# Kernel tuning notes

Measured on AMD Instinct MI355X. Metric: run time of the kernel, lower is better.

## Reference

```python
import jax, jax.numpy as jnp
import numpy as np

D_EMBED = 1024
N_HEADS = 16
BATCH = 2
SEQ = 2048


def setup_inputs() -> dict:
    key = jax.random.key(0)
    k1, k2, k3 = jax.random.split(key, 3)
    scale = 0.02
    x = jax.random.normal(k1, (BATCH, SEQ, D_EMBED), dtype=jnp.float32)
    w_qkv = jax.random.normal(k2, (D_EMBED, 3 * D_EMBED), dtype=jnp.float32) * scale
    b_qkv = jnp.zeros((3 * D_EMBED,), dtype=jnp.float32)
    w_o = jax.random.normal(k3, (D_EMBED, D_EMBED), dtype=jnp.float32) * scale
    b_o = jnp.zeros((D_EMBED,), dtype=jnp.float32)
    return {"x": x, "w_qkv": w_qkv, "b_qkv": b_qkv, "w_o": w_o, "b_o": b_o}


def reference(x, w_qkv, b_qkv, w_o, b_o):
    bs, sl, ed = x.shape
    nh = N_HEADS
    hd = ed // nh
    # fused QKV projection, split into q, k, v
    qkv = x @ w_qkv + b_qkv                      # [bs, sl, 3*ed]
    q, k, v = jnp.split(qkv, 3, axis=2)
    # [bs, sl, (nh hd)] -> [bs, nh, sl, hd]
    def heads(t):
        return t.reshape(bs, sl, nh, hd).transpose(0, 2, 1, 3)
    q, k, v = heads(q), heads(k), heads(v)
    # scaled dot-product attention with causal mask (full SxS scores, as in the original)
    scores = jnp.einsum('bhqd,bhkd->bhqk', q, k) / jnp.sqrt(jnp.float32(hd))
    causal = jnp.tril(jnp.ones((sl, sl), dtype=bool))
    scores = jnp.where(causal[None, None, :, :], scores, jnp.float32(-jnp.inf))
    attn = jax.nn.softmax(scores, axis=-1)       # dropout p=0 -> identity
    out = jnp.einsum('bhqk,bhkd->bhqd', attn, v) # [bs, nh, sl, hd]
    out = out.transpose(0, 2, 1, 3).reshape(bs, sl, ed)
    return out @ w_o + b_o
```

## Files before the change

kernel.cpp:

```cpp
#include <hip/hip_runtime.h>
#include <hip/hip_bf16.h>

typedef __hip_bfloat16 bf16;
typedef unsigned short u16;
typedef __attribute__((ext_vector_type(8))) short short8;
typedef __attribute__((ext_vector_type(4))) float floatx4;

#define D_EMBED 1024
#define N_HEADS 16
#define HEAD_DIM 64
#define BATCH 2
#define SEQ 2048
#define ROWS (BATCH * SEQ)
#define QKV_COLS (3 * D_EMBED)
#define QSCALE 0.1803368801f

__device__ __forceinline__ void g2l16(const void* g, void* l) {
    __builtin_amdgcn_global_load_lds(
        (const __attribute__((address_space(1))) unsigned int*)g,
        (__attribute__((address_space(3))) unsigned int*)l,
        16, 0, 0);
}

__device__ __forceinline__ u16 f2b_bits(float f) {
    bf16 h = __float2bfloat16(f);
    u16 u;
    __builtin_memcpy(&u, &h, 2);
    return u;
}

__device__ __forceinline__ unsigned pack2(float a, float b) {
    return (unsigned)f2b_bits(a) | ((unsigned)f2b_bits(b) << 16);
}

__device__ __forceinline__ float fexp2(float x) {
#if __has_builtin(__builtin_amdgcn_exp2f)
    return __builtin_amdgcn_exp2f(x);
#else
    return exp2f(x);
#endif
}

__device__ __forceinline__ unsigned permpack(float a, float b) {
#if __has_builtin(__builtin_amdgcn_perm)
    return __builtin_amdgcn_perm(__float_as_uint(b), __float_as_uint(a), 0x07060302u);
#else
    return (__float_as_uint(a) >> 16) | (__float_as_uint(b) & 0xFFFF0000u);
#endif
}

__global__ __launch_bounds__(256)
void prep(const float* __restrict__ x, const float* __restrict__ w_qkv,
          const float* __restrict__ w_o, bf16* __restrict__ xb,
          bf16* __restrict__ wqkvT, bf16* __restrict__ woT)
{
    __shared__ u16 T[64][72];
    const int tid = threadIdx.x;
    const int bid = blockIdx.x;

    if (bid < 4096) {
        const int i = bid * 256 + tid;
        const float4 v = reinterpret_cast<const float4*>(x)[i];
        ushort4 o;
        o.x = f2b_bits(v.x); o.y = f2b_bits(v.y);
        o.z = f2b_bits(v.z); o.w = f2b_bits(v.w);
        reinterpret_cast<ushort4*>(xb)[i] = o;
        return;
    }
    const float* in; u16* out; int R, C, bx, by;
    if (bid < 4864) {
        const int t = bid - 4096;
        in = w_qkv; out = reinterpret_cast<u16*>(wqkvT); R = 1024; C = 3072;
        bx = t % 48; by = t / 48;
    } else {
        const int t = bid - 4864;
        in = w_o; out = reinterpret_cast<u16*>(woT); R = 1024; C = 1024;
        bx = t % 16; by = t / 16;
    }
    const int r0 = by * 64, c0 = bx * 64;
#pragma unroll
    for (int it = 0; it < 4; ++it) {
        const int r = (tid >> 4) + it * 16;
        const int c4 = (tid & 15) * 4;
        const float4 v = *reinterpret_cast<const float4*>(in + (size_t)(r0 + r) * C + c0 + c4);
        T[c4 + 0][r] = f2b_bits(v.x);
        T[c4 + 1][r] = f2b_bits(v.y);
        T[c4 + 2][r] = f2b_bits(v.z);
        T[c4 + 3][r] = f2b_bits(v.w);
    }
    __syncthreads();
#pragma unroll
    for (int it = 0; it < 4; ++it) {
        const int rr = (tid >> 4) + it * 16;
        const int cc4 = (tid & 15) * 4;
        ushort4 o = *reinterpret_cast<const ushort4*>(&T[rr][cc4]);
        *reinterpret_cast<ushort4*>(out + (size_t)(c0 + rr) * R + r0 + cc4) = o;
    }
}

__global__ __launch_bounds__(256)
void gemm_qkv(const bf16* __restrict__ A, const bf16* __restrict__ Bt,
              const float* __restrict__ bias,
              bf16* __restrict__ qb, bf16* __restrict__ kb, bf16* __restrict__ vtb)
{
    __shared__ __align__(16) char smem[32768];
    char* BUF0 = smem;
    char* BUF1 = smem + 16384;

    const int tid = threadIdx.x;
    const int lane = tid & 63, w = tid >> 6;
    const int quad = lane >> 4, l15 = lane & 15;
    const int mw = (w >> 1) * 64, nw = (w & 1) * 64;
    const int blockM = blockIdx.y * 128, blockN = blockIdx.x * 128;

    const int row0 = tid >> 2, ch = tid & 3;
    const int off0 = (tid & ~63) * 16;
    const bf16* Asrc0 = A + (size_t)(blockM + row0) * 1024 + ch * 8;
    const bf16* Asrc1 = Asrc0 + (size_t)64 * 1024;
    const bf16* Bsrc0 = Bt + (size_t)(blockN + row0) * 1024 + ch * 8;
    const bf16* Bsrc1 = Bsrc0 + (size_t)64 * 1024;

    auto stage = [&](int k0, char* buf) {
        g2l16(Asrc0 + k0, buf + off0);
        g2l16(Asrc1 + k0, buf + off0 + 4096);
        g2l16(Bsrc0 + k0, buf + 8192 + off0);
        g2l16(Bsrc1 + k0, buf + 8192 + off0 + 4096);
    };

    floatx4 acc[4][4];
#pragma unroll
    for (int i = 0; i < 4; ++i)
#pragma unroll
        for (int j = 0; j < 4; ++j) acc[i][j] = (floatx4){0.f, 0.f, 0.f, 0.f};

    auto compute = [&](char* buf) {
        short8 af[4], bfr[4];
#pragma unroll
        for (int mi = 0; mi < 4; ++mi)
            af[mi] = *reinterpret_cast<const short8*>(
                buf + (mw + mi * 16 + l15) * 64 + quad * 16);
#pragma unroll
        for (int ni = 0; ni < 4; ++ni)
            bfr[ni] = *reinterpret_cast<const short8*>(
                buf + 8192 + (nw + ni * 16 + l15) * 64 + quad * 16);
#pragma unroll
        for (int mi = 0; mi < 4; ++mi)
#pragma unroll
            for (int ni = 0; ni < 4; ++ni)
                acc[mi][ni] = __builtin_amdgcn_mfma_f32_16x16x32_bf16(
                    af[mi], bfr[ni], acc[mi][ni], 0, 0, 0);
    };

    stage(0, BUF0);
    __syncthreads();
#pragma unroll 1
    for (int k0 = 0; k0 < 1024; k0 += 64) {
        if (k0 + 32 < 1024) stage(k0 + 32, BUF1);
        compute(BUF0);
        __syncthreads();
        if (k0 + 64 < 1024) stage(k0 + 64, BUF0);
        compute(BUF1);
        __syncthreads();
    }

    u16* W = reinterpret_cast<u16*>(smem + w * 2304);
    const bool isq = (blockN < 1024);
    const bool isv = (blockN >= 2048);

    float bvn[4];
#pragma unroll
    for (int ni = 0; ni < 4; ++ni) bvn[ni] = bias[blockN + nw + ni * 16 + l15];

    if (!isv) {
        bf16* dstbuf = isq ? qb : kb;
        const int coloff = blockN - (isq ? 0 : 1024);
#pragma unroll
        for (int mi = 0; mi < 4; ++mi) {
#pragma unroll
            for (int ni = 0; ni < 4; ++ni) {
#pragma unroll
                for (int r = 0; r < 4; ++r) {
                    float val = acc[mi][ni][r] + bvn[ni];
                    if (isq) val *= QSCALE;
                    W[(quad * 4 + r) * 72 + ni * 16 + l15] = f2b_bits(val);
                }
            }
#pragma unroll
            for (int half = 0; half < 2; ++half) {
                const int idx = half * 64 + lane;
                const int rowL = idx >> 3, chh = idx & 7;
                short8 v = *reinterpret_cast<const short8*>(W + rowL * 72 + chh * 8);
                const int grow = blockM + mw + mi * 16 + rowL;
                const int gcol = coloff + nw + chh * 8;
                *reinterpret_cast<short8*>(
                    reinterpret_cast<u16*>(dstbuf) + (size_t)grow * 1024 + gcol) = v;
            }
        }
    } else {
        const int col0 = blockN - 2048 + nw;
        const int h = col0 >> 6;
        const int bh = (blockM >> 11) * 16 + h;
        const int sb = (blockM & 2047) + mw;
        u16* vdst = reinterpret_cast<u16*>(vtb) + (size_t)bh * 64 * SEQ;
#pragma unroll
        for (int mi = 0; mi < 4; ++mi) {
#pragma unroll
            for (int ni = 0; ni < 4; ++ni) {
#pragma unroll
                for (int r = 0; r < 4; ++r)
                    W[(quad * 4 + r) * 72 + ni * 16 + l15] =
                        f2b_bits(acc[mi][ni][r] + bvn[ni]);
            }
#pragma unroll
            for (int mc = 0; mc < 2; ++mc) {
                u16 tmp[8];
#pragma unroll
                for (int e = 0; e < 8; ++e) tmp[e] = W[(mc * 8 + e) * 72 + lane];
                const int s = sb + mi * 16 + mc * 8;
                *reinterpret_cast<short8*>(vdst + (size_t)lane * SEQ + s) =
                    *reinterpret_cast<const short8*>(tmp);
            }
        }
    }
}

__global__ __launch_bounds__(256)
void gemm_out(const bf16* __restrict__ A, const bf16* __restrict__ Bt,
              const float* __restrict__ bias, float* __restrict__ outf)
{
    __shared__ __align__(16) char smem[24576];
    char* BUF0 = smem;
    char* BUF1 = smem + 12288;

    const int tid = threadIdx.x;
    const int lane = tid & 63, w = tid >> 6;
    const int quad = lane >> 4, l15 = lane & 15;
    const int mw = (w >> 1) * 64, nw = (w & 1) * 32;
    const int blockM = blockIdx.y * 128, blockN = blockIdx.x * 64;

    const int row0 = tid >> 2, ch = tid & 3;
    const int off0 = (tid & ~63) * 16;
    const bf16* Asrc0 = A + (size_t)(blockM + row0) * 1024 + ch * 8;
    const bf16* Asrc1 = Asrc0 + (size_t)64 * 1024;
    const bf16* Bsrc0 = Bt + (size_t)(blockN + row0) * 1024 + ch * 8;

    auto stage = [&](int k0, char* buf) {
        g2l16(Asrc0 + k0, buf + off0);
        g2l16(Asrc1 + k0, buf + off0 + 4096);
        g2l16(Bsrc0 + k0, buf + 8192 + off0);
    };

    floatx4 acc[4][2];
#pragma unroll
    for (int i = 0; i < 4; ++i)
#pragma unroll
        for (int j = 0; j < 2; ++j) acc[i][j] = (floatx4){0.f, 0.f, 0.f, 0.f};

    auto compute = [&](char* buf) {
        short8 af[4], bfr[2];
#pragma unroll
        for (int mi = 0; mi < 4; ++mi)
            af[mi] = *reinterpret_cast<const short8*>(
                buf + (mw + mi * 16 + l15) * 64 + quad * 16);
#pragma unroll
        for (int ni = 0; ni < 2; ++ni)
            bfr[ni] = *reinterpret_cast<const short8*>(
                buf + 8192 + (nw + ni * 16 + l15) * 64 + quad * 16);
#pragma unroll
        for (int mi = 0; mi < 4; ++mi)
#pragma unroll
            for (int ni = 0; ni < 2; ++ni)
                acc[mi][ni] = __builtin_amdgcn_mfma_f32_16x16x32_bf16(
                    af[mi], bfr[ni], acc[mi][ni], 0, 0, 0);
    };

    stage(0, BUF0);
    __syncthreads();
#pragma unroll 1
    for (int k0 = 0; k0 < 1024; k0 += 64) {
        if (k0 + 32 < 1024) stage(k0 + 32, BUF1);
        compute(BUF0);
        __syncthreads();
        if (k0 + 64 < 1024) stage(k0 + 64, BUF0);
        compute(BUF1);
        __syncthreads();
    }

    float bvn[2];
#pragma unroll
    for (int ni = 0; ni < 2; ++ni) bvn[ni] = bias[blockN + nw + ni * 16 + l15];

#pragma unroll
    for (int mi = 0; mi < 4; ++mi)
#pragma unroll
        for (int r = 0; r < 4; ++r) {
            const int row = blockM + mw + mi * 16 + quad * 4 + r;
#pragma unroll
            for (int ni = 0; ni < 2; ++ni) {
                const int col = blockN + nw + ni * 16 + l15;
                outf[(size_t)row * 1024 + col] = acc[mi][ni][r] + bvn[ni];
            }
        }
}

__global__ __launch_bounds__(256)
void attn_mfma(const bf16* __restrict__ qb, const bf16* __restrict__ kb,
               const bf16* __restrict__ vtb, bf16* __restrict__ ob)
{
    __shared__ __align__(16) char smem[81920];
    char* A0 = smem;
    char* A1 = smem + 16384;
    char* B0 = smem + 32768;
    char* B1 = smem + 49152;
    const int tid = threadIdx.x;
    const int lane = tid & 63, w = tid >> 6;
    const int quad = lane >> 4, l15 = lane & 15;
    char* PsB = smem + 65536 + w * 2048;
    char* PsS = smem + 73728 + w * 2048;

    const int l = blockIdx.x;
    const int bh = l & 31;
    const int slot = l >> 5;
    const int pi = (slot < 8) ? slot : 23 - slot;
    const int b = bh >> 4, h = bh & 15;

    const int qtS = pi, qtB = 31 - pi;
    const int q0S = qtS * 64, q0B = qtB * 64;
    const int KT = qtB + 1;
    const int qrowS = q0S + w * 16 + l15;
    const int qrowB = q0B + w * 16 + l15;

    const size_t kvrow = (size_t)b * SEQ;
    const size_t vbase = (size_t)bh * 64 * SEQ;

    const short8 ones = {0x3F80, 0x3F80, 0x3F80, 0x3F80,
                         0x3F80, 0x3F80, 0x3F80, 0x3F80};

    const int row0 = tid >> 3;
    const int lch = (tid & 7) ^ (row0 & 7);
    const int loff0 = (tid & ~63) * 16;
    const int loff1 = loff0 + 4096;
    const bf16* ksrc0 = kb + (kvrow + row0) * D_EMBED + h * 64 + lch * 8;
    const bf16* ksrc1 = ksrc0 + (size_t)32 * D_EMBED;
    const bf16* vsrc0 = vtb + vbase + (size_t)row0 * SEQ + lch * 8;
    const bf16* vsrc1 = vsrc0 + (size_t)32 * SEQ;

    auto prefetch = [&](int nkt, char* dst) {
        const size_t ko = (size_t)nkt * 64;
        g2l16(ksrc0 + ko * D_EMBED, dst + loff0);
        g2l16(ksrc1 + ko * D_EMBED, dst + loff1);
        g2l16(vsrc0 + ko, dst + 8192 + loff0);
        g2l16(vsrc1 + ko, dst + 8192 + loff1);
    };

    {
        const bf16* qsrcS = qb + (kvrow + q0S + row0) * D_EMBED + h * 64 + lch * 8;
        const bf16* qsrcB = qb + (kvrow + q0B + row0) * D_EMBED + h * 64 + lch * 8;
        g2l16(qsrcS, B0 + loff0);
        g2l16(qsrcS + (size_t)32 * D_EMBED, B0 + loff1);
        g2l16(qsrcB, B0 + 8192 + loff0);
        g2l16(qsrcB + (size_t)32 * D_EMBED, B0 + 8192 + loff1);
        prefetch(0, A0);
        prefetch(1, A1);
    }
    __syncthreads();

    const int qoff = (w * 16 + l15) * 128;
    const int x0 = (quad ^ (l15 & 7)) * 16;
    const int x1 = ((quad + 4) ^ (l15 & 7)) * 16;
    const short8 qS0 = *reinterpret_cast<const short8*>(B0 + qoff + x0);
    const short8 qS1 = *reinterpret_cast<const short8*>(B0 + qoff + x1);
    const short8 qB0 = *reinterpret_cast<const short8*>(B0 + 8192 + qoff + x0);
    const short8 qB1 = *reinterpret_cast<const short8*>(B0 + 8192 + qoff + x1);
    __syncthreads();

    floatx4 OaccS[4], OaccB[4], LaccS, LaccB;
#pragma unroll
    for (int i = 0; i < 4; ++i) {
        OaccS[i] = (floatx4){0.f, 0.f, 0.f, 0.f};
        OaccB[i] = (floatx4){0.f, 0.f, 0.f, 0.f};
    }
    LaccS = (floatx4){0.f, 0.f, 0.f, 0.f};
    LaccB = (floatx4){0.f, 0.f, 0.f, 0.f};

    auto compute = [&](int kt, char* Ks, char* Vs) {
        const int k0 = kt * 64;
        const bool doS = (kt <= qtS);
        short8 kf[2][4], vf[2][4];
#pragma unroll
        for (int ms = 0; ms < 4; ++ms) {
            const int roff = (ms * 16 + l15) * 128;
            kf[0][ms] = *reinterpret_cast<const short8*>(Ks + roff + x0);
            kf[1][ms] = *reinterpret_cast<const short8*>(Ks + roff + x1);
        }
#pragma unroll
        for (int ks = 0; ks < 2; ++ks)
#pragma unroll
            for (int ds = 0; ds < 4; ++ds)
                vf[ks][ds] = *reinterpret_cast<const short8*>(
                    Vs + (ds * 16 + l15) * 128 + (((quad + ks * 4) ^ (l15 & 7)) * 16));

        floatx4 SB[4], SS[4];
        __builtin_amdgcn_s_setprio(1);
#pragma unroll
        for (int ms = 0; ms < 4; ++ms) {
            floatx4 t = (floatx4){0.f, 0.f, 0.f, 0.f};
            t = __builtin_amdgcn_mfma_f32_16x16x32_bf16(kf[0][ms], qB0, t, 0, 0, 0);
            SB[ms] = __builtin_amdgcn_mfma_f32_16x16x32_bf16(kf[1][ms], qB1, t, 0, 0, 0);
        }
        if (doS) {
#pragma unroll
            for (int ms = 0; ms < 4; ++ms) {
                floatx4 t = (floatx4){0.f, 0.f, 0.f, 0.f};
                t = __builtin_amdgcn_mfma_f32_16x16x32_bf16(kf[0][ms], qS0, t, 0, 0, 0);
                SS[ms] = __builtin_amdgcn_mfma_f32_16x16x32_bf16(kf[1][ms], qS1, t, 0, 0, 0);
            }
        }
        __builtin_amdgcn_s_setprio(0);

        const bool diagB = (kt == KT - 1);
#pragma unroll
        for (int ms = 0; ms < 4; ++ms) {
            float p[4];
#pragma unroll
            for (int r = 0; r < 4; ++r) {
                float s = SB[ms][r];
                if (diagB && (k0 + ms * 16 + quad * 4 + r) > qrowB) s = -1e30f;
                p[r] = fexp2(s);
            }
            const int k = ms * 16 + quad * 4;
            uint2 pw;
            pw.x = permpack(p[0], p[1]);
            pw.y = permpack(p[2], p[3]);
            *reinterpret_cast<uint2*>(PsB + (k >> 3) * 256 + l15 * 16 + (k & 7) * 2) = pw;
        }
        if (doS) {
            const bool diagS = (kt == qtS);
#pragma unroll
            for (int ms = 0; ms < 4; ++ms) {
                float p[4];
#pragma unroll
                for (int r = 0; r < 4; ++r) {
                    float s = SS[ms][r];
                    if (diagS && (k0 + ms * 16 + quad * 4 + r) > qrowS) s = -1e30f;
                    p[r] = fexp2(s);
                }
                const int k = ms * 16 + quad * 4;
                uint2 pw;
                pw.x = permpack(p[0], p[1]);
                pw.y = permpack(p[2], p[3]);
                *reinterpret_cast<uint2*>(PsS + (k >> 3) * 256 + l15 * 16 + (k & 7) * 2) = pw;
            }
        }

        __builtin_amdgcn_s_setprio(1);
#pragma unroll
        for (int ks = 0; ks < 2; ++ks) {
            const short8 pfB = *reinterpret_cast<const short8*>(
                PsB + (ks * 4 + quad) * 256 + l15 * 16);
            LaccB = __builtin_amdgcn_mfma_f32_16x16x32_bf16(ones, pfB, LaccB, 0, 0, 0);
#pragma unroll
            for (int ds = 0; ds < 4; ++ds)
                OaccB[ds] = __builtin_amdgcn_mfma_f32_16x16x32_bf16(
                    vf[ks][ds], pfB, OaccB[ds], 0, 0, 0);
            if (doS) {
                const short8 pfS = *reinterpret_cast<const short8*>(
                    PsS + (ks * 4 + quad) * 256 + l15 * 16);
                LaccS = __builtin_amdgcn_mfma_f32_16x16x32_bf16(ones, pfS, LaccS, 0, 0, 0);
#pragma unroll
                for (int ds = 0; ds < 4; ++ds)
                    OaccS[ds] = __builtin_amdgcn_mfma_f32_16x16x32_bf16(
                        vf[ks][ds], pfS, OaccS[ds], 0, 0, 0);
            }
        }
        __builtin_amdgcn_s_setprio(0);
    };

#pragma unroll 1
    for (int kt = 0; kt < KT; kt += 4) {
        if (kt + 2 < KT) prefetch(kt + 2, B0);
        if (kt + 3 < KT) prefetch(kt + 3, B1);
        compute(kt, A0, A0 + 8192);
        if (kt + 1 < KT) compute(kt + 1, A1, A1 + 8192);
        __syncthreads();
        if (kt + 2 >= KT) break;
        if (kt + 4 < KT) prefetch(kt + 4, A0);
        if (kt + 5 < KT) prefetch(kt + 5, A1);
        compute(kt + 2, B0, B0 + 8192);
        if (kt + 3 < KT) compute(kt + 3, B1, B1 + 8192);
        __syncthreads();
    }

#pragma unroll
    for (int which = 0; which < 2; ++which) {
        const floatx4* Oacc = which ? OaccB : OaccS;
        const float invl = 1.f / (which ? LaccB[0] : LaccS[0]);
        const int q0 = which ? q0B : q0S;
#pragma unroll
        for (int ds = 0; ds < 4; ++ds) {
            const int d = ds * 16 + quad * 4;
            uint2 ow;
            ow.x = pack2(Oacc[ds][0] * invl, Oacc[ds][1] * invl);
            ow.y = pack2(Oacc[ds][2] * invl, Oacc[ds][3] * invl);
            *reinterpret_cast<uint2*>(
                PsB + (d >> 3) * 256 + l15 * 16 + (d & 7) * 2) = ow;
        }
#pragma unroll
        for (int it = 0; it < 2; ++it) {
            const int idx = it * 64 + lane;
            const int chh = idx >> 4, q = idx & 15;
            short8 ov = *reinterpret_cast<const short8*>(PsB + chh * 256 + q * 16);
            *reinterpret_cast<short8*>(
                ob + (kvrow + q0 + w * 16 + q) * D_EMBED + h * 64 + chh * 8) = ov;
        }
    }
}

extern "C" void kernel_launch(void* const* d_in, const int* in_sizes, int n_in,
                              void* d_out, int out_size, void* d_ws, size_t ws_size,
                              hipStream_t stream)
{
    const float* x     = (const float*)d_in[0];
    const float* w_qkv = (const float*)d_in[1];
    const float* b_qkv = (const float*)d_in[2];
    const float* w_o   = (const float*)d_in[3];
    const float* b_o   = (const float*)d_in[4];
    float* out = (float*)d_out;

    bf16* xb     = (bf16*)d_ws;
    bf16* wqkvT  = xb + (size_t)4096 * 1024;
    bf16* woT    = wqkvT + (size_t)3072 * 1024;
    bf16* qbuf   = woT + (size_t)1024 * 1024;
    bf16* kbuf   = qbuf + (size_t)4096 * 1024;
    bf16* vtb    = kbuf + (size_t)4096 * 1024;
    bf16* attnb  = vtb + (size_t)4096 * 1024;

    dim3 blk(256);

    prep<<<dim3(5120), blk, 0, stream>>>(x, w_qkv, w_o, xb, wqkvT, woT);

    gemm_qkv<<<dim3(24, 32), blk, 0, stream>>>(xb, wqkvT, b_qkv, qbuf, kbuf, vtb);

    attn_mfma<<<dim3(512), blk, 0, stream>>>(qbuf, kbuf, vtb, attnb);

    gemm_out<<<dim3(16, 32), blk, 0, stream>>>(attnb, woT, b_o, out);
}
```

Measured before the change: 172.9 us.

## Split attention block into separate waves for big and small query tiles

The attention kernel goes from 256 to 512 threads per block. Waves 0-3 now handle the large (late) query tile and waves 4-7 the small (early) one, where each wave used to compute both. Each thread issues half as many global-to-LDS loads and holds half the accumulators, which lowers register pressure and doubles the waves available to hide latency. The cost is load imbalance: the small-tile waves finish their causal range early and then sit idle at the block barriers.

```diff
diff --git a/kernel.cpp b/kernel.cpp
--- a/kernel.cpp
+++ b/kernel.cpp
@@ -303,7 +303,7 @@
         }
 }
 
-__global__ __launch_bounds__(256)
+__global__ __launch_bounds__(512)
 void attn_mfma(const bf16* __restrict__ qb, const bf16* __restrict__ kb,
                const bf16* __restrict__ vtb, bf16* __restrict__ ob)
 {
@@ -315,8 +315,7 @@
     const int tid = threadIdx.x;
     const int lane = tid & 63, w = tid >> 6;
     const int quad = lane >> 4, l15 = lane & 15;
-    char* PsB = smem + 65536 + w * 2048;
-    char* PsS = smem + 73728 + w * 2048;
+    char* Ps = smem + 65536 + w * 2048;
 
     const int l = blockIdx.x;
     const int bh = l & 31;
@@ -327,8 +326,9 @@
     const int qtS = pi, qtB = 31 - pi;
     const int q0S = qtS * 64, q0B = qtB * 64;
     const int KT = qtB + 1;
-    const int qrowS = q0S + w * 16 + l15;
-    const int qrowB = q0B + w * 16 + l15;
+    const bool isB = (w < 4);
+    const int qrow = (isB ? q0B : q0S) + (w & 3) * 16 + l15;
+    const int diagKT = isB ? (KT - 1) : qtS;
 
     const size_t kvrow = (size_t)b * SEQ;
     const size_t vbase = (size_t)bh * 64 * SEQ;
@@ -338,54 +338,43 @@
 
     const int row0 = tid >> 3;
     const int lch = (tid & 7) ^ (row0 & 7);
-    const int loff0 = (tid & ~63) * 16;
-    const int loff1 = loff0 + 4096;
-    const bf16* ksrc0 = kb + (kvrow + row0) * D_EMBED + h * 64 + lch * 8;
-    const bf16* ksrc1 = ksrc0 + (size_t)32 * D_EMBED;
-    const bf16* vsrc0 = vtb + vbase + (size_t)row0 * SEQ + lch * 8;
-    const bf16* vsrc1 = vsrc0 + (size_t)32 * SEQ;
+    const int loff = (tid & ~63) * 16;
+    const bf16* ksrc = kb + (kvrow + row0) * D_EMBED + h * 64 + lch * 8;
+    const bf16* vsrc = vtb + vbase + (size_t)row0 * SEQ + lch * 8;
 
     auto prefetch = [&](int nkt, char* dst) {
         const size_t ko = (size_t)nkt * 64;
-        g2l16(ksrc0 + ko * D_EMBED, dst + loff0);
-        g2l16(ksrc1 + ko * D_EMBED, dst + loff1);
-        g2l16(vsrc0 + ko, dst + 8192 + loff0);
-        g2l16(vsrc1 + ko, dst + 8192 + loff1);
+        g2l16(ksrc + ko * D_EMBED, dst + loff);
+        g2l16(vsrc + ko, dst + 8192 + loff);
     };
 
     {
         const bf16* qsrcS = qb + (kvrow + q0S + row0) * D_EMBED + h * 64 + lch * 8;
         const bf16* qsrcB = qb + (kvrow + q0B + row0) * D_EMBED + h * 64 + lch * 8;
-        g2l16(qsrcS, B0 + loff0);
-        g2l16(qsrcS + (size_t)32 * D_EMBED, B0 + loff1);
-        g2l16(qsrcB, B0 + 8192 + loff0);
-        g2l16(qsrcB + (size_t)32 * D_EMBED, B0 + 8192 + loff1);
+        g2l16(qsrcS, B0 + loff);
+        g2l16(qsrcB, B0 + 8192 + loff);
         prefetch(0, A0);
         prefetch(1, A1);
     }
     __syncthreads();
 
-    const int qoff = (w * 16 + l15) * 128;
+    const int qoff = ((w & 3) * 16 + l15) * 128;
     const int x0 = (quad ^ (l15 & 7)) * 16;
     const int x1 = ((quad + 4) ^ (l15 & 7)) * 16;
-    const short8 qS0 = *reinterpret_cast<const short8*>(B0 + qoff + x0);
-    const short8 qS1 = *reinterpret_cast<const short8*>(B0 + qoff + x1);
-    const short8 qB0 = *reinterpret_cast<const short8*>(B0 + 8192 + qoff + x0);
-    const short8 qB1 = *reinterpret_cast<const short8*>(B0 + 8192 + qoff + x1);
+    const char* qbase = isB ? (B0 + 8192) : B0;
+    const short8 qf0 = *reinterpret_cast<const short8*>(qbase + qoff + x0);
+    const short8 qf1 = *reinterpret_cast<const short8*>(qbase + qoff + x1);
     __syncthreads();
 
-    floatx4 OaccS[4], OaccB[4], LaccS, LaccB;
-#pragma unroll
-    for (int i = 0; i < 4; ++i) {
-        OaccS[i] = (floatx4){0.f, 0.f, 0.f, 0.f};
-        OaccB[i] = (floatx4){0.f, 0.f, 0.f, 0.f};
-    }
-    LaccS = (floatx4){0.f, 0.f, 0.f, 0.f};
-    LaccB = (floatx4){0.f, 0.f, 0.f, 0.f};
+    floatx4 Oacc[4], Lacc;
+#pragma unroll
+    for (int i = 0; i < 4; ++i) Oacc[i] = (floatx4){0.f, 0.f, 0.f, 0.f};
+    Lacc = (floatx4){0.f, 0.f, 0.f, 0.f};
 
     auto compute = [&](int kt, char* Ks, char* Vs) {
+        const bool doMe = isB || (kt <= qtS);
+        if (!doMe) return;
         const int k0 = kt * 64;
-        const bool doS = (kt <= qtS);
         short8 kf[2][4], vf[2][4];
 #pragma unroll
         for (int ms = 0; ms < 4; ++ms) {
@@ -400,78 +389,43 @@
                 vf[ks][ds] = *reinterpret_cast<const short8*>(
                     Vs + (ds * 16 + l15) * 128 + (((quad + ks * 4) ^ (l15 & 7)) * 16));
 
-        floatx4 SB[4], SS[4];
+        floatx4 S[4];
         __builtin_amdgcn_s_setprio(1);
 #pragma unroll
         for (int ms = 0; ms < 4; ++ms) {
             floatx4 t = (floatx4){0.f, 0.f, 0.f, 0.f};
-            t = __builtin_amdgcn_mfma_f32_16x16x32_bf16(kf[0][ms], qB0, t, 0, 0, 0);
-            SB[ms] = __builtin_amdgcn_mfma_f32_16x16x32_bf16(kf[1][ms], qB1, t, 0, 0, 0);
-        }
-        if (doS) {
-#pragma unroll
-            for (int ms = 0; ms < 4; ++ms) {
-                floatx4 t = (floatx4){0.f, 0.f, 0.f, 0.f};
-                t = __builtin_amdgcn_mfma_f32_16x16x32_bf16(kf[0][ms], qS0, t, 0, 0, 0);
-                SS[ms] = __builtin_amdgcn_mfma_f32_16x16x32_bf16(kf[1][ms], qS1, t, 0, 0, 0);
-            }
+            t = __builtin_amdgcn_mfma_f32_16x16x32_bf16(kf[0][ms], qf0, t, 0, 0, 0);
+            S[ms] = __builtin_amdgcn_mfma_f32_16x16x32_bf16(kf[1][ms], qf1, t, 0, 0, 0);
         }
         __builtin_amdgcn_s_setprio(0);
 
-        const bool diagB = (kt == KT - 1);
+        const bool diag = (kt == diagKT);
 #pragma unroll
         for (int ms = 0; ms < 4; ++ms) {
             float p[4];
 #pragma unroll
             for (int r = 0; r < 4; ++r) {
-                float s = SB[ms][r];
-                if (diagB && (k0 + ms * 16 + quad * 4 + r) > qrowB) s = -1e30f;
+                float s = S[ms][r];
+                if (diag && (k0 + ms * 16 + quad * 4 + r) > qrow) s = -1e30f;
                 p[r] = fexp2(s);
             }
             const int k = ms * 16 + quad * 4;
             uint2 pw;
             pw.x = permpack(p[0], p[1]);
             pw.y = permpack(p[2], p[3]);
-            *reinterpret_cast<uint2*>(PsB + (k >> 3) * 256 + l15 * 16 + (k & 7) * 2) = pw;
-        }
-        if (doS) {
-            const bool diagS = (kt == qtS);
-#pragma unroll
-            for (int ms = 0; ms < 4; ++ms) {
-                float p[4];
-#pragma unroll
-                for (int r = 0; r < 4; ++r) {
-                    float s = SS[ms][r];
-                    if (diagS && (k0 + ms * 16 + quad * 4 + r) > qrowS) s = -1e30f;
-                    p[r] = fexp2(s);
-                }
-                const int k = ms * 16 + quad * 4;
-                uint2 pw;
-                pw.x = permpack(p[0], p[1]);
-                pw.y = permpack(p[2], p[3]);
-                *reinterpret_cast<uint2*>(PsS + (k >> 3) * 256 + l15 * 16 + (k & 7) * 2) = pw;
-            }
+            *reinterpret_cast<uint2*>(Ps + (k >> 3) * 256 + l15 * 16 + (k & 7) * 2) = pw;
         }
 
         __builtin_amdgcn_s_setprio(1);
 #pragma unroll
         for (int ks = 0; ks < 2; ++ks) {
-            const short8 pfB = *reinterpret_cast<const short8*>(
-                PsB + (ks * 4 + quad) * 256 + l15 * 16);
-            LaccB = __builtin_amdgcn_mfma_f32_16x16x32_bf16(ones, pfB, LaccB, 0, 0, 0);
+            const short8 pf = *reinterpret_cast<const short8*>(
+                Ps + (ks * 4 + quad) * 256 + l15 * 16);
+            Lacc = __builtin_amdgcn_mfma_f32_16x16x32_bf16(ones, pf, Lacc, 0, 0, 0);
 #pragma unroll
             for (int ds = 0; ds < 4; ++ds)
-                OaccB[ds] = __builtin_amdgcn_mfma_f32_16x16x32_bf16(
-                    vf[ks][ds], pfB, OaccB[ds], 0, 0, 0);
-            if (doS) {
-                const short8 pfS = *reinterpret_cast<const short8*>(
-                    PsS + (ks * 4 + quad) * 256 + l15 * 16);
-                LaccS = __builtin_amdgcn_mfma_f32_16x16x32_bf16(ones, pfS, LaccS, 0, 0, 0);
-#pragma unroll
-                for (int ds = 0; ds < 4; ++ds)
-                    OaccS[ds] = __builtin_amdgcn_mfma_f32_16x16x32_bf16(
-                        vf[ks][ds], pfS, OaccS[ds], 0, 0, 0);
-            }
+                Oacc[ds] = __builtin_amdgcn_mfma_f32_16x16x32_bf16(
+                    vf[ks][ds], pf, Oacc[ds], 0, 0, 0);
         }
         __builtin_amdgcn_s_setprio(0);
     };
@@ -491,11 +445,9 @@
         __syncthreads();
     }
 
-#pragma unroll
-    for (int which = 0; which < 2; ++which) {
-        const floatx4* Oacc = which ? OaccB : OaccS;
-        const float invl = 1.f / (which ? LaccB[0] : LaccS[0]);
-        const int q0 = which ? q0B : q0S;
+    {
+        const float invl = 1.f / Lacc[0];
+        const int q0w = (isB ? q0B : q0S) + (w & 3) * 16;
 #pragma unroll
         for (int ds = 0; ds < 4; ++ds) {
             const int d = ds * 16 + quad * 4;
@@ -503,15 +455,15 @@
             ow.x = pack2(Oacc[ds][0] * invl, Oacc[ds][1] * invl);
             ow.y = pack2(Oacc[ds][2] * invl, Oacc[ds][3] * invl);
             *reinterpret_cast<uint2*>(
-                PsB + (d >> 3) * 256 + l15 * 16 + (d & 7) * 2) = ow;
+                Ps + (d >> 3) * 256 + l15 * 16 + (d & 7) * 2) = ow;
         }
 #pragma unroll
         for (int it = 0; it < 2; ++it) {
             const int idx = it * 64 + lane;
             const int chh = idx >> 4, q = idx & 15;
-            short8 ov = *reinterpret_cast<const short8*>(PsB + chh * 256 + q * 16);
+            short8 ov = *reinterpret_cast<const short8*>(Ps + chh * 256 + q * 16);
             *reinterpret_cast<short8*>(
-                ob + (kvrow + q0 + w * 16 + q) * D_EMBED + h * 64 + chh * 8) = ov;
+                ob + (kvrow + q0w + q) * D_EMBED + h * 64 + chh * 8) = ov;
         }
     }
 }
@@ -541,7 +493,7 @@
 
     gemm_qkv<<<dim3(24, 32), blk, 0, stream>>>(xb, wqkvT, b_qkv, qbuf, kbuf, vtb);
 
-    attn_mfma<<<dim3(512), blk, 0, stream>>>(qbuf, kbuf, vtb, attnb);
+    attn_mfma<<<dim3(512), dim3(512), 0, stream>>>(qbuf, kbuf, vtb, attnb);
 
     gemm_out<<<dim3(16, 32), blk, 0, stream>>>(attnb, woT, b_o, out);
 }
```

Measured after the change: 173.5 us. About the same (+0.4%).
